# Optimization experiments

Measured on AMD Instinct MI355X. Metric: run time of the kernel, lower is better.

## Reference

```python
import jax, jax.numpy as jnp
import numpy as np

BJORCK_BETA = 0.5
BJORCK_ITERS = 25

def bjorck_orthonormalize(w, iters=BJORCK_ITERS):
    # Order-2 Bjorck iteration (beta must be 0.5):
    # w <- 15/8 * w - 5/4 * w (w^T w) + 3/8 * w (w^T w)^2
    def body(i, w):
        wtw = w.T @ w                     # [out, out] on the thin side
        wtw2 = wtw @ wtw
        return 1.875 * w - 1.25 * (w @ wtw) + 0.375 * (w @ wtw2)
    return jax.lax.fori_loop(0, iters, body, w)

def setup_inputs() -> dict:
    key = jax.random.key(0)
    k1, k2, k3 = jax.random.split(key, 3)
    N, D_IN, D_OUT = 8192, 512, 256
    x = jax.random.normal(k1, (N, D_IN), dtype=jnp.float32)
    adj = jax.random.uniform(k2, (N, N), dtype=jnp.float32)
    weight = jax.random.normal(k3, (D_OUT, D_IN), dtype=jnp.float32) / np.sqrt(D_IN)
    return {"x": x, "adj": adj, "weight": weight}

def reference(x, adj, weight):
    # safe Bjorck scaling: sqrt(rows * cols) of the weight (shape-only constant)
    scaling = jnp.sqrt(jnp.float32(weight.shape[0] * weight.shape[1]))
    # orthonormalize weight.T / scaling, then transpose back -> [out, in]
    ortho_w = bjorck_orthonormalize(weight.T / scaling).T
    h = x @ ortho_w.T                      # [N, out] == F.linear(x, ortho_w)
    return jax.nn.relu(adj @ h)            # [N, out]
```

## Files before the change

### kernel.cpp

```cpp
#include <hip/hip_runtime.h>

typedef __attribute__((ext_vector_type(8))) short bf16x8;
typedef __attribute__((ext_vector_type(4))) short bf16x4;
typedef __attribute__((ext_vector_type(4))) float f32x4;

__device__ __forceinline__ unsigned short f2bf(float x){
  unsigned u = __float_as_uint(x);
  u = (u + 0x7fffu + ((u >> 16) & 1u)) >> 16;
  return (unsigned short)u;
}

__device__ __forceinline__ bf16x8 cvtpack8(float4 a, float4 b){
  union { bf16x8 v; unsigned short u[8]; } p;
  p.u[0] = f2bf(a.x); p.u[1] = f2bf(a.y); p.u[2] = f2bf(a.z); p.u[3] = f2bf(a.w);
  p.u[4] = f2bf(b.x); p.u[5] = f2bf(b.y); p.u[6] = f2bf(b.z); p.u[7] = f2bf(b.w);
  return p.v;
}

__device__ __forceinline__ void gload16(const void* g, void* l){
  __builtin_amdgcn_global_load_lds(
      (const __attribute__((address_space(1))) unsigned int*)g,
      (__attribute__((address_space(3))) unsigned int*)l, 16, 0, 0);
}


__global__ __launch_bounds__(256) void kzero(float* __restrict__ G0, float* __restrict__ n2){
  int b = blockIdx.x;
  if (b < 256) G0[b * 256 + threadIdx.x] = 0.0f;
  else if (threadIdx.x == 0) *n2 = 0.0f;
}


__global__ __launch_bounds__(256) void knorm(const float* __restrict__ wt, float* __restrict__ n2){
  int t = blockIdx.x * 256 + threadIdx.x;
  float4 v = reinterpret_cast<const float4*>(wt)[t];
  float s = v.x*v.x + v.y*v.y + v.z*v.z + v.w*v.w;
  #pragma unroll
  for (int o = 32; o > 0; o >>= 1) s += __shfl_down(s, o, 64);
  __shared__ float red[4];
  if ((threadIdx.x & 63) == 0) red[threadIdx.x >> 6] = s;
  __syncthreads();
  if (threadIdx.x == 0) atomicAdd(n2, red[0] + red[1] + red[2] + red[3]);
}

__global__ __launch_bounds__(256) void kinit(const float* __restrict__ wt, const float* __restrict__ n2,
                                             float* __restrict__ W){
  int c = blockIdx.x;
  int r = threadIdx.x;
  float s = rsqrtf(*n2) * (1.0f / 0.3f);
  W[(size_t)r * 256 + c]         = wt[(size_t)c * 512 + r] * s;
  W[(size_t)(r + 256) * 256 + c] = wt[(size_t)c * 512 + r + 256] * s;
}

__global__ __launch_bounds__(256) void kgram2(const float* __restrict__ W, float* __restrict__ G){
  __shared__ __align__(16) float Wi[64][32];
  __shared__ __align__(16) float Wj[64][32];
  const int t = threadIdx.x;
  const int i0 = blockIdx.y * 32, j0 = blockIdx.x * 32, k0 = blockIdx.z * 64;
  const int lr = t >> 3, lc = (t & 7) * 4;
  #pragma unroll
  for (int p = 0; p < 2; ++p){
    int r = lr + p * 32;
    *reinterpret_cast<float4*>(&Wi[r][lc]) =
        *reinterpret_cast<const float4*>(&W[(size_t)(k0 + r) * 256 + i0 + lc]);
    *reinterpret_cast<float4*>(&Wj[r][lc]) =
        *reinterpret_cast<const float4*>(&W[(size_t)(k0 + r) * 256 + j0 + lc]);
  }
  __syncthreads();
  const int tx = t & 31, iy = t >> 5;
  float g0 = 0, g1 = 0, g2 = 0, g3 = 0;
  #pragma unroll 8
  for (int k = 0; k < 64; ++k){
    float wj = Wj[k][tx];
    float4 wi = *reinterpret_cast<const float4*>(&Wi[k][iy * 4]);
    g0 = fmaf(wi.x, wj, g0); g1 = fmaf(wi.y, wj, g1);
    g2 = fmaf(wi.z, wj, g2); g3 = fmaf(wi.w, wj, g3);
  }
  float* gp = &G[(size_t)(i0 + iy * 4) * 256 + j0 + tx];
  atomicAdd(gp,       g0); atomicAdd(gp + 256, g1);
  atomicAdd(gp + 512, g2); atomicAdd(gp + 768, g3);
}

__global__ __launch_bounds__(512) void kupdate2(float* __restrict__ W, const float* __restrict__ G,
    float* __restrict__ Gnext, float ca, float cb, float cc, int last,
    unsigned short* __restrict__ WT2){
  __shared__ float wr[2][256], yl[2][256];
  const int t = threadIdx.x;
  const int c = t & 255, row = t >> 8;
  const int r = blockIdx.x * 2 + row;
  wr[row][c] = W[(size_t)r * 256 + c];
  __syncthreads();
  float y = 0;
  #pragma unroll 8
  for (int k = 0; k < 256; ++k)
    y = fmaf(wr[row][k], G[(size_t)k * 256 + c], y);
  yl[row][c] = y;
  __syncthreads();
  float d = 0;
  #pragma unroll 8
  for (int k = 0; k < 256; ++k)
    d = fmaf(yl[row][k], G[(size_t)k * 256 + c], d);
  float nw = ca * wr[row][c] + cb * y + cc * d;
  W[(size_t)r * 256 + c] = nw;
  if (r < 256) Gnext[(size_t)r * 256 + c] = 0.0f;
  if (last){
    size_t e = (size_t)(r >> 5) * 8192 + (size_t)((r >> 3) & 3) * 2048 + (size_t)c * 8 + (r & 7);
    WT2[e] = f2bf(nw);
  }
}

template<int KDIM, int KS, int EPI>
__global__ __launch_bounds__(256) void kgemmS(const float* __restrict__ A,
    const unsigned short* __restrict__ B, void* __restrict__ Cout){
  __shared__ __align__(16) unsigned short As[2][4096];
  __shared__ __align__(16) unsigned short Bs[2][8192];

  const int t = threadIdx.x;
  const int w = t >> 6, lane = t & 63;
  const int rlo = lane & 15, l16 = lane >> 4;
  const int kp = (KS > 1) ? (int)(blockIdx.x % KS) : 0;
  const int rb = (KS > 1) ? (int)(blockIdx.x / KS) : (int)blockIdx.x;
  constexpr int KLOC = KDIM / KS;
  constexpr int NS = KLOC / 32;
  const int kbase = kp * KLOC;

  const int arow = t >> 1, akh = t & 1;
  const float* astg = A + (size_t)(rb * 128 + arow) * KDIM + kbase + akh * 16;
  const int aswz = (arow >> 1) & 3;
  const int ab0 = arow * 64 + ((2 * akh)     ^ aswz) * 16;
  const int ab1 = arow * 64 + ((2 * akh + 1) ^ aswz) * 16;
  const unsigned short* bstg = B + (size_t)(kbase >> 5) * 8192 + w * 2048 + lane * 8;

  f32x4 acc[2][16];
  #pragma unroll
  for (int mf = 0; mf < 2; ++mf)
    #pragma unroll
    for (int nf = 0; nf < 16; ++nf){
      acc[mf][nf][0] = 0.f; acc[mf][nf][1] = 0.f;
      acc[mf][nf][2] = 0.f; acc[mf][nf][3] = 0.f;
    }

  float4 q0, q1, q2, q3;
#define LOADA(S) { const float* p_ = astg + (size_t)(S) * 32; \
    q0 = *reinterpret_cast<const float4*>(p_); \
    q1 = *reinterpret_cast<const float4*>(p_ + 4); \
    q2 = *reinterpret_cast<const float4*>(p_ + 8); \
    q3 = *reinterpret_cast<const float4*>(p_ + 12); }
#define WRITEA(BUF) { char* b_ = reinterpret_cast<char*>(&As[BUF][0]); \
    *reinterpret_cast<bf16x8*>(b_ + ab0) = cvtpack8(q0, q1); \
    *reinterpret_cast<bf16x8*>(b_ + ab1) = cvtpack8(q2, q3); }
#define STAGE_B(BUF, S) { \
    _Pragma("unroll") \
    for (int i = 0; i < 4; ++i) \
      gload16(bstg + (size_t)(S) * 8192 + i * 512, &Bs[BUF][w * 2048 + i * 512]); }
#define COMPUTE(BUF) { \
    bf16x8 afr[2]; \
    const char* ab_ = reinterpret_cast<const char*>(&As[BUF][0]); \
    _Pragma("unroll") \
    for (int mf = 0; mf < 2; ++mf){ \
      int row = w * 32 + mf * 16 + rlo; \
      afr[mf] = *reinterpret_cast<const bf16x8*>( \
          ab_ + row * 64 + ((l16 ^ ((row >> 1) & 3)) * 16)); \
    } \
    _Pragma("unroll") \
    for (int nf = 0; nf < 16; ++nf){ \
      bf16x8 bf_ = *reinterpret_cast<const bf16x8*>(&Bs[BUF][l16 * 2048 + (nf * 16 + rlo) * 8]); \
      acc[0][nf] = __builtin_amdgcn_mfma_f32_16x16x32_bf16(afr[0], bf_, acc[0][nf], 0, 0, 0); \
      acc[1][nf] = __builtin_amdgcn_mfma_f32_16x16x32_bf16(afr[1], bf_, acc[1][nf], 0, 0, 0); \
    } }

  STAGE_B(0, 0);
  LOADA(0);
  WRITEA(0);
  __syncthreads();

  #pragma unroll 1
  for (int s = 0; s < NS; ++s){
    const int cur = s & 1;
    if (s + 1 < NS){ STAGE_B(cur ^ 1, s + 1); LOADA(s + 1); }
    COMPUTE(cur);
    if (s + 1 < NS) WRITEA(cur ^ 1);
    __syncthreads();
  }
#undef LOADA
#undef WRITEA
#undef STAGE_B
#undef COMPUTE

  if constexpr (EPI == 0){
    unsigned short* H = reinterpret_cast<unsigned short*>(Cout);
    #pragma unroll
    for (int mf = 0; mf < 2; ++mf)
      #pragma unroll
      for (int nf = 0; nf < 16; ++nf){
        int c  = nf * 16 + rlo;
        int m0 = rb * 128 + w * 32 + mf * 16 + (l16 << 2);
        size_t e = (size_t)(m0 >> 5) * 8192 + (size_t)((m0 >> 3) & 3) * 2048
                 + (size_t)c * 8 + (m0 & 7);
        union { bf16x4 v; unsigned short u[4]; } p;
        p.u[0] = f2bf(acc[mf][nf][0]);
        p.u[1] = f2bf(acc[mf][nf][1]);
        p.u[2] = f2bf(acc[mf][nf][2]);
        p.u[3] = f2bf(acc[mf][nf][3]);
        *reinterpret_cast<bf16x4*>(&H[e]) = p.v;
      }
  } else {
    float* O = reinterpret_cast<float*>(Cout) + (size_t)kp * 8192 * 256;
    #pragma unroll
    for (int mf = 0; mf < 2; ++mf)
      #pragma unroll
      for (int nf = 0; nf < 16; ++nf){
        int c  = nf * 16 + rlo;
        int m0 = rb * 128 + w * 32 + mf * 16 + (l16 << 2);
        #pragma unroll
        for (int j = 0; j < 4; ++j)
          O[(size_t)(m0 + j) * 256 + c] = acc[mf][nf][j];
      }
  }
}

template<int KDIM, int KS>
__global__ __launch_bounds__(512) void kgemmF(const float* __restrict__ A,
    const unsigned short* __restrict__ B, float* __restrict__ Cout){
  __shared__ __align__(16) unsigned short Bs[3][8192];

  const int t = threadIdx.x;
  const int w = t >> 6, lane = t & 63;
  const int rlo = lane & 15, l16 = lane >> 4;
  const int kp = (int)(blockIdx.x % KS);
  const int rb = (int)(blockIdx.x / KS);
  constexpr int KLOC = KDIM / KS;
  constexpr int NS = KLOC / 32;
  const int kbase = kp * KLOC;

  const int row0 = rb * 256 + w * 32 + rlo;
  const float* a0 = A + (size_t)row0 * KDIM + kbase + l16 * 8;
  const float* a1 = a0 + (size_t)16 * KDIM;
  const unsigned short* bstg = B + (size_t)(kbase >> 5) * 8192 + w * 1024 + lane * 8;

  f32x4 acc[2][16];
  #pragma unroll
  for (int mf = 0; mf < 2; ++mf)
    #pragma unroll
    for (int nf = 0; nf < 16; ++nf){
      acc[mf][nf][0] = 0.f; acc[mf][nf][1] = 0.f;
      acc[mf][nf][2] = 0.f; acc[mf][nf][3] = 0.f;
    }

#define LDA(Q, S) { const float* pa_ = a0 + (size_t)(S) * 32; \
    const float* pb_ = a1 + (size_t)(S) * 32; \
    Q[0] = *reinterpret_cast<const float4*>(pa_); \
    Q[1] = *reinterpret_cast<const float4*>(pa_ + 4); \
    Q[2] = *reinterpret_cast<const float4*>(pb_); \
    Q[3] = *reinterpret_cast<const float4*>(pb_ + 4); }
#define STB(BUF, S) { \
    _Pragma("unroll") \
    for (int i = 0; i < 2; ++i) \
      gload16(bstg + (size_t)(S) * 8192 + i * 512, &Bs[BUF][w * 1024 + i * 512]); }
#define STEP(PB, Q, S) { \
    bf16x8 bfr[16]; \
    _Pragma("unroll") \
    for (int nf = 0; nf < 16; ++nf) \
      bfr[nf] = *reinterpret_cast<const bf16x8*>(&Bs[PB][l16 * 2048 + (nf * 16 + rlo) * 8]); \
    bf16x8 afr0 = cvtpack8(Q[0], Q[1]); \
    bf16x8 afr1 = cvtpack8(Q[2], Q[3]); \
    { int st_ = ((S) + 2 < NS) ? (S) + 2 : NS - 1; \
      int pn_ = (PB) + 2; if (pn_ >= 3) pn_ -= 3; \
      LDA(Q, st_); \
      STB(pn_, st_); } \
    _Pragma("unroll") \
    for (int nf = 0; nf < 16; ++nf){ \
      acc[0][nf] = __builtin_amdgcn_mfma_f32_16x16x32_bf16(afr0, bfr[nf], acc[0][nf], 0, 0, 0); \
      acc[1][nf] = __builtin_amdgcn_mfma_f32_16x16x32_bf16(afr1, bfr[nf], acc[1][nf], 0, 0, 0); \
    } \
    asm volatile("s_waitcnt vmcnt(6)" ::: "memory"); \
    __builtin_amdgcn_s_barrier(); \
    asm volatile("" ::: "memory"); }

  float4 q0[4], q1[4];
  STB(0, 0);
  STB(1, 1);
  LDA(q0, 0);
  LDA(q1, 1);
  asm volatile("s_waitcnt vmcnt(4)" ::: "memory");
  __builtin_amdgcn_s_barrier();
  asm volatile("" ::: "memory");

  int p = 0;
  #pragma unroll 1
  for (int s = 0; s < NS; s += 2){
    int p1 = p + 1; if (p1 >= 3) p1 -= 3;
    STEP(p, q0, s);
    STEP(p1, q1, s + 1);
    p = p1 + 1; if (p >= 3) p -= 3;
  }
#undef LDA
#undef STB
#undef STEP

  float* O = Cout + (size_t)kp * 8192 * 256;
  #pragma unroll
  for (int mf = 0; mf < 2; ++mf)
    #pragma unroll
    for (int nf = 0; nf < 16; ++nf){
      int c  = nf * 16 + rlo;
      int m0 = rb * 256 + w * 32 + mf * 16 + (l16 << 2);
      #pragma unroll
      for (int j = 0; j < 4; ++j)
        O[(size_t)(m0 + j) * 256 + c] = acc[mf][nf][j];
    }
}

__global__ __launch_bounds__(256) void kreduce8(const float* __restrict__ P, float* __restrict__ O){
  size_t i = (size_t)blockIdx.x * 256 + threadIdx.x;
  const float4* p = reinterpret_cast<const float4*>(P);
  float4 r = p[i];
  #pragma unroll
  for (int q = 1; q < 8; ++q){
    float4 b = p[i + (size_t)q * 524288];
    r.x += b.x; r.y += b.y; r.z += b.z; r.w += b.w;
  }
  r.x = fmaxf(r.x, 0.f); r.y = fmaxf(r.y, 0.f);
  r.z = fmaxf(r.z, 0.f); r.w = fmaxf(r.w, 0.f);
  reinterpret_cast<float4*>(O)[i] = r;
}


extern "C" void kernel_launch(void* const* d_in, const int* in_sizes, int n_in,
                              void* d_out, int out_size, void* d_ws, size_t ws_size,
                              hipStream_t stream) {
  const float* x   = (const float*)d_in[0];
  const float* adj = (const float*)d_in[1];
  const float* wt  = (const float*)d_in[2];
  float* out = (float*)d_out;

  char* ws = (char*)d_ws;
  float* n2            = (float*)ws;
  float* W             = (float*)(ws + 4096);
  float* G0            = (float*)(ws + 4096 + 524288);
  float* G1            = (float*)(ws + 4096 + 524288 + 262144);
  unsigned short* WT2  = (unsigned short*)(ws + 4096 + 524288 + 2*262144);
  unsigned short* HT2  = (unsigned short*)(ws + 4096 + 524288 + 3*262144);
  float* Cpart         = (float*)(ws + 4096 + 524288 + 3*262144 + 4194304);

  kzero<<<257, 256, 0, stream>>>(G0, n2);
  knorm<<<128, 256, 0, stream>>>(wt, n2);
  kinit<<<256, 256, 0, stream>>>(wt, n2, W);

  const float ca[4] = { 4.2000f, 3.4445f, 1.875f, 1.875f };
  const float cb[4] = {-9.0000f, -4.7750f, -1.25f, -1.25f };
  const float cc[4] = {-6.8000f, 2.0315f, 0.375f, 0.375f };
  float* Gb[2] = {G0, G1};
  for (int it = 0; it < 4; ++it){
    float* Gc = Gb[it & 1];
    float* Gn = Gb[(it + 1) & 1];
    kgram2<<<dim3(8, 8, 8), 256, 0, stream>>>(W, Gc);
    kupdate2<<<256, 512, 0, stream>>>(W, Gc, Gn, ca[it], cb[it], cc[it], it == 3 ? 1 : 0, WT2);
  }

  kgemmS<512, 1, 0><<<64, 256, 0, stream>>>(x, WT2, (void*)HT2);
  kgemmF<8192, 8><<<256, 512, 0, stream>>>(adj, HT2, Cpart);
  kreduce8<<<2048, 256, 0, stream>>>(Cpart, out);
}
```

Baseline: 238.1 us.

## Tile Bjorck update through LDS and swizzle bf16 B layout for GEMMs

Rewrites the Bjorck update kernel so each block handles 8 rows, stages G tiles in LDS and computes 4 outputs per thread with float4 loads. This replaces the repeated uncoalesced global reads of G. It also adds a rotation swizzle to the packed bf16 B layout (WT2/HT2 writers and the GEMM readers) to cut LDS bank conflicts. The big GEMM now interleaves its B fragment loads with the MFMAs and sets a launch bound of one block per CU. The smaller update grid uses fewer blocks, and the swizzle must match on both the writer and reader sides.

```diff
diff --git a/kernel.cpp b/kernel.cpp
--- a/kernel.cpp
+++ b/kernel.cpp
@@ -81,31 +81,80 @@
   atomicAdd(gp + 512, g2); atomicAdd(gp + 768, g3);
 }
 
-__global__ __launch_bounds__(512) void kupdate2(float* __restrict__ W, const float* __restrict__ G,
+__global__ __launch_bounds__(512) void kupdate3(float* __restrict__ W, const float* __restrict__ G,
     float* __restrict__ Gnext, float ca, float cb, float cc, int last,
     unsigned short* __restrict__ WT2){
-  __shared__ float wr[2][256], yl[2][256];
+  __shared__ __align__(16) float wl[8][256];
+  __shared__ __align__(16) float Gt[64][256];
+  __shared__ __align__(16) float yl[8][256];
   const int t = threadIdx.x;
-  const int c = t & 255, row = t >> 8;
-  const int r = blockIdx.x * 2 + row;
-  wr[row][c] = W[(size_t)r * 256 + c];
+  const int row = t >> 6;
+  const int c0  = (t & 63) * 4;
+  const int rg  = blockIdx.x * 8 + row;
+
+  *reinterpret_cast<float4*>(&wl[row][c0]) =
+      *reinterpret_cast<const float4*>(&W[(size_t)rg * 256 + c0]);
+
+  float y0 = 0, y1 = 0, y2 = 0, y3 = 0;
+  for (int kt = 0; kt < 4; ++kt){
+    __syncthreads();
+    #pragma unroll
+    for (int i = 0; i < 8; ++i){
+      int idx = (i * 512 + t) * 4;
+      int r = idx >> 8, c = idx & 255;
+      *reinterpret_cast<float4*>(&Gt[r][c]) =
+          *reinterpret_cast<const float4*>(&G[(size_t)(kt * 64 + r) * 256 + c]);
+    }
+    __syncthreads();
+    #pragma unroll 4
+    for (int k = 0; k < 64; ++k){
+      float wv = wl[row][kt * 64 + k];
+      float4 g = *reinterpret_cast<const float4*>(&Gt[k][c0]);
+      y0 = fmaf(wv, g.x, y0); y1 = fmaf(wv, g.y, y1);
+      y2 = fmaf(wv, g.z, y2); y3 = fmaf(wv, g.w, y3);
+    }
+  }
   __syncthreads();
-  float y = 0;
-  #pragma unroll 8
-  for (int k = 0; k < 256; ++k)
-    y = fmaf(wr[row][k], G[(size_t)k * 256 + c], y);
-  yl[row][c] = y;
-  __syncthreads();
-  float d = 0;
-  #pragma unroll 8
-  for (int k = 0; k < 256; ++k)
-    d = fmaf(yl[row][k], G[(size_t)k * 256 + c], d);
-  float nw = ca * wr[row][c] + cb * y + cc * d;
-  W[(size_t)r * 256 + c] = nw;
-  if (r < 256) Gnext[(size_t)r * 256 + c] = 0.0f;
+  yl[row][c0] = y0; yl[row][c0+1] = y1; yl[row][c0+2] = y2; yl[row][c0+3] = y3;
+
+  float d0 = 0, d1 = 0, d2 = 0, d3 = 0;
+  for (int kt = 0; kt < 4; ++kt){
+    __syncthreads();
+    #pragma unroll
+    for (int i = 0; i < 8; ++i){
+      int idx = (i * 512 + t) * 4;
+      int r = idx >> 8, c = idx & 255;
+      *reinterpret_cast<float4*>(&Gt[r][c]) =
+          *reinterpret_cast<const float4*>(&G[(size_t)(kt * 64 + r) * 256 + c]);
+    }
+    __syncthreads();
+    #pragma unroll 4
+    for (int k = 0; k < 64; ++k){
+      float yv = yl[row][kt * 64 + k];
+      float4 g = *reinterpret_cast<const float4*>(&Gt[k][c0]);
+      d0 = fmaf(yv, g.x, d0); d1 = fmaf(yv, g.y, d1);
+      d2 = fmaf(yv, g.z, d2); d3 = fmaf(yv, g.w, d3);
+    }
+  }
+
+  float4 wv = *reinterpret_cast<const float4*>(&wl[row][c0]);
+  float4 nw;
+  nw.x = ca * wv.x + cb * y0 + cc * d0;
+  nw.y = ca * wv.y + cb * y1 + cc * d1;
+  nw.z = ca * wv.z + cb * y2 + cc * d2;
+  nw.w = ca * wv.w + cb * y3 + cc * d3;
+  *reinterpret_cast<float4*>(&W[(size_t)rg * 256 + c0]) = nw;
+  if (rg < 256){
+    float4 z = {0.f, 0.f, 0.f, 0.f};
+    *reinterpret_cast<float4*>(&Gnext[(size_t)rg * 256 + c0]) = z;
+  }
   if (last){
-    size_t e = (size_t)(r >> 5) * 8192 + (size_t)((r >> 3) & 3) * 2048 + (size_t)c * 8 + (r & 7);
-    WT2[e] = f2bf(nw);
+    int g = (rg >> 3) & 3;
+    size_t base = (size_t)(rg >> 5) * 8192 + (size_t)g * 2048;
+    float v[4] = {nw.x, nw.y, nw.z, nw.w};
+    #pragma unroll
+    for (int j = 0; j < 4; ++j)
+      WT2[base + (size_t)(((c0 + j) + 2 * g) & 255) * 8 + (rg & 7)] = f2bf(v[j]);
   }
 }
 
@@ -164,7 +213,8 @@
     } \
     _Pragma("unroll") \
     for (int nf = 0; nf < 16; ++nf){ \
-      bf16x8 bf_ = *reinterpret_cast<const bf16x8*>(&Bs[BUF][l16 * 2048 + (nf * 16 + rlo) * 8]); \
+      bf16x8 bf_ = *reinterpret_cast<const bf16x8*>( \
+          &Bs[BUF][l16 * 2048 + (((nf * 16 + rlo) + 2 * l16) & 255) * 8]); \
       acc[0][nf] = __builtin_amdgcn_mfma_f32_16x16x32_bf16(afr[0], bf_, acc[0][nf], 0, 0, 0); \
       acc[1][nf] = __builtin_amdgcn_mfma_f32_16x16x32_bf16(afr[1], bf_, acc[1][nf], 0, 0, 0); \
     } }
@@ -195,8 +245,9 @@
       for (int nf = 0; nf < 16; ++nf){
         int c  = nf * 16 + rlo;
         int m0 = rb * 128 + w * 32 + mf * 16 + (l16 << 2);
-        size_t e = (size_t)(m0 >> 5) * 8192 + (size_t)((m0 >> 3) & 3) * 2048
-                 + (size_t)c * 8 + (m0 & 7);
+        int g  = (m0 >> 3) & 3;
+        size_t e = (size_t)(m0 >> 5) * 8192 + (size_t)g * 2048
+                 + (size_t)((c + 2 * g) & 255) * 8 + (m0 & 7);
         union { bf16x4 v; unsigned short u[4]; } p;
         p.u[0] = f2bf(acc[mf][nf][0]);
         p.u[1] = f2bf(acc[mf][nf][1]);
@@ -220,7 +271,7 @@
 }
 
 template<int KDIM, int KS>
-__global__ __launch_bounds__(512) void kgemmF(const float* __restrict__ A,
+__global__ __launch_bounds__(512, 1) void kgemmF2(const float* __restrict__ A,
     const unsigned short* __restrict__ B, float* __restrict__ Cout){
   __shared__ __align__(16) unsigned short Bs[3][8192];
 
@@ -258,10 +309,6 @@
     for (int i = 0; i < 2; ++i) \
       gload16(bstg + (size_t)(S) * 8192 + i * 512, &Bs[BUF][w * 1024 + i * 512]); }
 #define STEP(PB, Q, S) { \
-    bf16x8 bfr[16]; \
-    _Pragma("unroll") \
-    for (int nf = 0; nf < 16; ++nf) \
-      bfr[nf] = *reinterpret_cast<const bf16x8*>(&Bs[PB][l16 * 2048 + (nf * 16 + rlo) * 8]); \
     bf16x8 afr0 = cvtpack8(Q[0], Q[1]); \
     bf16x8 afr1 = cvtpack8(Q[2], Q[3]); \
     { int st_ = ((S) + 2 < NS) ? (S) + 2 : NS - 1; \
@@ -269,9 +316,15 @@
       LDA(Q, st_); \
       STB(pn_, st_); } \
     _Pragma("unroll") \
-    for (int nf = 0; nf < 16; ++nf){ \
-      acc[0][nf] = __builtin_amdgcn_mfma_f32_16x16x32_bf16(afr0, bfr[nf], acc[0][nf], 0, 0, 0); \
-      acc[1][nf] = __builtin_amdgcn_mfma_f32_16x16x32_bf16(afr1, bfr[nf], acc[1][nf], 0, 0, 0); \
+    for (int nf = 0; nf < 16; nf += 2){ \
+      bf16x8 b0 = *reinterpret_cast<const bf16x8*>( \
+          &Bs[PB][l16 * 2048 + (((nf * 16 + rlo) + 2 * l16) & 255) * 8]); \
+      bf16x8 b1 = *reinterpret_cast<const bf16x8*>( \
+          &Bs[PB][l16 * 2048 + ((((nf + 1) * 16 + rlo) + 2 * l16) & 255) * 8]); \
+      acc[0][nf]   = __builtin_amdgcn_mfma_f32_16x16x32_bf16(afr0, b0, acc[0][nf], 0, 0, 0); \
+      acc[1][nf]   = __builtin_amdgcn_mfma_f32_16x16x32_bf16(afr1, b0, acc[1][nf], 0, 0, 0); \
+      acc[0][nf+1] = __builtin_amdgcn_mfma_f32_16x16x32_bf16(afr0, b1, acc[0][nf+1], 0, 0, 0); \
+      acc[1][nf+1] = __builtin_amdgcn_mfma_f32_16x16x32_bf16(afr1, b1, acc[1][nf+1], 0, 0, 0); \
     } \
     asm volatile("s_waitcnt vmcnt(6)" ::: "memory"); \
     __builtin_amdgcn_s_barrier(); \
@@ -355,10 +408,10 @@
     float* Gc = Gb[it & 1];
     float* Gn = Gb[(it + 1) & 1];
     kgram2<<<dim3(8, 8, 8), 256, 0, stream>>>(W, Gc);
-    kupdate2<<<256, 512, 0, stream>>>(W, Gc, Gn, ca[it], cb[it], cc[it], it == 3 ? 1 : 0, WT2);
+    kupdate3<<<64, 512, 0, stream>>>(W, Gc, Gn, ca[it], cb[it], cc[it], it == 3 ? 1 : 0, WT2);
   }
 
   kgemmS<512, 1, 0><<<64, 256, 0, stream>>>(x, WT2, (void*)HT2);
-  kgemmF<8192, 8><<<256, 512, 0, stream>>>(adj, HT2, Cpart);
+  kgemmF2<8192, 8><<<256, 512, 0, stream>>>(adj, HT2, Cpart);
   kreduce8<<<2048, 256, 0, stream>>>(Cpart, out);
 }
```

New measurement: 239.3 us. About the same (+0.5%).
